# Kernel tuning notes

Measured on AMD Instinct MI355X. Metric: run time of the kernel, lower is better.

The kernel has to match this reference:

```python
import jax, jax.numpy as jnp
import numpy as np

B, S, DM = 1, 2048, 2048
H, KV, DH = 32, 8, 64
ROT, DQ = 32, 16  # rotary dims; DQ = ROT // 2
GROUPS = H // KV


def setup_inputs() -> dict:
    key = jax.random.key(0)
    ks = jax.random.split(key, 9)
    sc = 0.02
    hidden_states = jax.random.normal(ks[0], (B, S, DM), jnp.float32)
    # realistic RoPE tables: theta = pos * inv_freq, shape [1,1,S,DQ] (broadcasts over heads)
    inv_freq = 1.0 / (10000.0 ** (jnp.arange(DQ, dtype=jnp.float32) / DQ))
    ang = jnp.arange(S, dtype=jnp.float32)[:, None] * inv_freq[None, :]
    cos = jnp.cos(ang)[None, None]
    sin = jnp.sin(ang)[None, None]
    position_ids = jnp.broadcast_to(jnp.arange(S, dtype=jnp.int64 if jax.config.read('jax_enable_x64') else jnp.int32), (B, S))
    Wq = jax.random.normal(ks[1], (DM, H * DH), jnp.float32) * sc
    Wk = jax.random.normal(ks[2], (DM, KV * DH), jnp.float32) * sc
    Wv = jax.random.normal(ks[3], (DM, KV * DH), jnp.float32) * sc
    Wo = jax.random.normal(ks[4], (H * DH, DM), jnp.float32) * sc
    qkv_dim = H * DH + 2 * KV * DH
    tau_Wq = jax.random.normal(ks[5], (qkv_dim, H), jnp.float32) * sc
    tau_Wv = jax.random.normal(ks[6], (qkv_dim, H), jnp.float32) * sc
    tau_alpha = jax.random.normal(ks[7], (H,), jnp.float32)
    return {"hidden_states": hidden_states, "cos": cos, "sin": sin,
            "position_ids": position_ids, "Wq": Wq, "Wk": Wk, "Wv": Wv,
            "Wo": Wo, "tau_Wq": tau_Wq, "tau_Wv": tau_Wv, "tau_alpha": tau_alpha}


def _rope(x, cos, sin):
    # x: [B, h, S, DH]; rotate first ROT dims (half-split real/imag), interleave output
    x_rot, x_pass = x[..., :ROT], x[..., ROT:]
    xr, xi = x_rot[..., :DQ], x_rot[..., DQ:]
    out_r = xr * cos - xi * sin
    out_i = xr * sin + xi * cos
    out = jnp.stack([out_r, out_i], axis=-1).reshape(x.shape[:-1] + (ROT,))
    return jnp.concatenate([out, x_pass], axis=-1)


def reference(hidden_states, cos, sin, position_ids, Wq, Wk, Wv, Wo, tau_Wq, tau_Wv, tau_alpha):
    b, s, _ = hidden_states.shape
    q = hidden_states @ Wq                      # [B,S,H*DH]
    k = hidden_states @ Wk                      # [B,S,KV*DH]
    v = hidden_states @ Wv                      # [B,S,KV*DH]
    # tau gating: gelu(concat qkv) -> tanh projections -> position sigmoid term
    feat = jax.nn.gelu(jnp.concatenate([q, k, v], axis=-1), approximate=False)
    tok_q = jnp.tanh(feat @ tau_Wq).transpose(0, 2, 1)   # [B,H,S]
    tok_v = jnp.tanh(feat @ tau_Wv).transpose(0, 2, 1)   # [B,H,S]
    pos = position_ids.astype(hidden_states.dtype) + 1.0
    tau_pos = 1.0 + (jax.nn.sigmoid(tau_alpha[None, :, None] * jnp.log(pos)[:, None, :]) - 0.5)
    tau_q = (tok_q + tau_pos)[..., None]        # [B,H,S,1]
    tau_v = (tok_v + tau_pos)[..., None]        # [B,H,S,1]
    q = q.reshape(b, s, H, DH).transpose(0, 2, 1, 3) * tau_q   # [B,H,S,DH]
    k = k.reshape(b, s, KV, DH).transpose(0, 2, 1, 3)          # [B,KV,S,DH]
    # torch: tau_v.repeat(1,groups,1,1)[:, :KV] == first KV heads of tau_v
    v = v.reshape(b, s, KV, DH).transpose(0, 2, 1, 3) * tau_v[:, :KV]
    q = _rope(q, cos, sin)
    k = _rope(k, cos, sin)
    # GQA expand kv heads, causal SDPA
    k = jnp.repeat(k, GROUPS, axis=1)
    v = jnp.repeat(v, GROUPS, axis=1)
    scores = jnp.einsum('bhqd,bhkd->bhqk', q, k) / np.sqrt(DH).astype(np.float32)
    causal = jnp.tril(jnp.ones((s, s), dtype=bool))
    scores = jnp.where(causal, scores, jnp.finfo(scores.dtype).min)
    attn = jax.nn.softmax(scores, axis=-1)
    out = jnp.einsum('bhqk,bhkd->bhqd', attn, v)
    out = out.transpose(0, 2, 1, 3).reshape(b, s, H * DH)
    return out @ Wo
```

## Files before the change

kernel.cpp:

```cpp
#include <hip/hip_runtime.h>
#include <cmath>

typedef __bf16 bf16x8 __attribute__((ext_vector_type(8)));
typedef __bf16 bf16x4 __attribute__((ext_vector_type(4)));
typedef float f32x4 __attribute__((ext_vector_type(4)));
typedef short s16x4 __attribute__((ext_vector_type(4)));
typedef unsigned short u16;
typedef unsigned int u32;

__device__ __forceinline__ u16 f2bf(float f) {
  union { float f; unsigned int u; } v; v.f = f;
  unsigned int u = v.u;
  return (u16)((u + 0x7FFFu + ((u >> 16) & 1u)) >> 16);
}

__device__ __forceinline__ float geluf(float x) {
  return 0.5f * x * (1.0f + erff(x * 0.7071067811865475f));
}

__device__ __forceinline__ f32x4 mfma_16x16x16_bf16(s16x4 a, s16x4 b, f32x4 c) {
#if __has_builtin(__builtin_amdgcn_mfma_f32_16x16x16bf16_1k)
  return __builtin_amdgcn_mfma_f32_16x16x16bf16_1k(a, b, c, 0, 0, 0);
#else
  f32x4 d;
  asm volatile("v_mfma_f32_16x16x16_bf16 %0, %1, %2, %3"
               : "=v"(d) : "v"(a), "v"(b), "0"(c));
  return d;
#endif
}

__device__ __forceinline__ void gl_lds16(const void* g, void* l) {
  __builtin_amdgcn_global_load_lds(
      (const __attribute__((address_space(1))) u32*)g,
      (__attribute__((address_space(3))) u32*)l, 16, 0, 0);
}

__global__ __launch_bounds__(256) void cvt_bf16(const float* __restrict__ in,
                                                u16* __restrict__ out, int n8) {
  int i = blockIdx.x * 256 + threadIdx.x;
  if (i >= n8) return;
  const float4* p = (const float4*)in + 2 * (size_t)i;
  float4 a = p[0], b = p[1];
  uint4 o;
  o.x = (unsigned)f2bf(a.x) | ((unsigned)f2bf(a.y) << 16);
  o.y = (unsigned)f2bf(a.z) | ((unsigned)f2bf(a.w) << 16);
  o.z = (unsigned)f2bf(b.x) | ((unsigned)f2bf(b.y) << 16);
  o.w = (unsigned)f2bf(b.z) | ((unsigned)f2bf(b.w) << 16);
  ((uint4*)out)[i] = o;
}

__global__ __launch_bounds__(256) void transpose_all(const float* __restrict__ Wq,
                                                     const float* __restrict__ Wk,
                                                     const float* __restrict__ Wv,
                                                     const float* __restrict__ Wo,
                                                     const float* __restrict__ tWq,
                                                     const float* __restrict__ tWv,
                                                     u16* __restrict__ WqkvT,
                                                     u16* __restrict__ WoT,
                                                     u16* __restrict__ Tt) {
  __shared__ float tile[64][65];
  int b = blockIdx.x;
  const float* in; u16* out; int R, C, bx, by;
  if (b < 1024)      { in = Wq;  out = WqkvT;                R = 2048; C = 2048; bx = b & 31; by = b >> 5; }
  else if (b < 1280) { b -= 1024; in = Wk; out = WqkvT + 2048ull * 2048; R = 2048; C = 512; bx = b & 7; by = b >> 3; }
  else if (b < 1536) { b -= 1280; in = Wv; out = WqkvT + 2560ull * 2048; R = 2048; C = 512; bx = b & 7; by = b >> 3; }
  else if (b < 2560) { b -= 1536; in = Wo; out = WoT;        R = 2048; C = 2048; bx = b & 31; by = b >> 5; }
  else if (b < 2608) { b -= 2560; in = tWq; out = Tt;               R = 3072; C = 32; bx = 0; by = b; }
  else               { b -= 2608; in = tWv; out = Tt + 32ull * 3072; R = 3072; C = 32; bx = 0; by = b; }

  const int t = threadIdx.x;
  const int r0 = by * 64, c0 = bx * 64;
  const int lr = t >> 4, lc4 = (t & 15) * 4;
#pragma unroll
  for (int p = 0; p < 4; ++p) {
    int r = p * 16 + lr;
    float4 v = {0.f, 0.f, 0.f, 0.f};
    if (c0 + lc4 < C) v = *(const float4*)(in + (size_t)(r0 + r) * C + c0 + lc4);
    tile[r][lc4] = v.x; tile[r][lc4 + 1] = v.y;
    tile[r][lc4 + 2] = v.z; tile[r][lc4 + 3] = v.w;
  }
  __syncthreads();
  const int cg = t >> 4, rr4 = (t & 15) * 4;
#pragma unroll
  for (int p = 0; p < 4; ++p) {
    int c = p * 16 + cg;
    if (c0 + c < C) {
      uint2 w;
      w.x = (u32)f2bf(tile[rr4][c])     | ((u32)f2bf(tile[rr4 + 1][c]) << 16);
      w.y = (u32)f2bf(tile[rr4 + 2][c]) | ((u32)f2bf(tile[rr4 + 3][c]) << 16);
      *(uint2*)(out + (size_t)(c0 + c) * R + r0 + rr4) = w;
    }
  }
}

template <int WR, int WC>
__global__ __launch_bounds__(256, 3) void gemm_bt(const u16* __restrict__ A,
                                                  const u16* __restrict__ Bt,
                                                  float* __restrict__ Cpart,
                                                  int M, int N, int K, int kPer) {
  constexpr int BM = WR * 64, BN = WC * 64;
  __shared__ __attribute__((aligned(16))) u16 As[BM * 64];
  __shared__ __attribute__((aligned(16))) u16 Bs[BN * 64];
  const int tid = threadIdx.x, wid = tid >> 6, lane = tid & 63;
  const int l16 = lane & 15, quad = lane >> 4;
  const int wm = (wid % WR) * 64, wn = (wid / WR) * 64;
  const int m0 = blockIdx.y * BM, n0 = blockIdx.x * BN;
  const int kIters = K >> 6;
  const int kStart = blockIdx.z * kPer;
  const int kEnd = (kStart + kPer < kIters) ? (kStart + kPer) : kIters;

  const int lrow = lane >> 3;
  const int swz = (lane & 7) ^ lrow;
  const u16* gAb = A + (size_t)m0 * K + (size_t)swz * 8;
  const u16* gBb = Bt + (size_t)n0 * K + (size_t)swz * 8;
  const int sx = l16 & 7;

  f32x4 acc[4][4] = {};
  for (int kt = kStart; kt < kEnd; ++kt) {
    __syncthreads();
    const u16* gA = gAb + (size_t)kt * 64;
    const u16* gB = gBb + (size_t)kt * 64;
#pragma unroll
    for (int j = 0; j < BM / 32; ++j) {
      int i = wid * (BM / 32) + j;
      gl_lds16(gA + (size_t)(i * 8 + lrow) * K, &As[i * 512]);
    }
#pragma unroll
    for (int j = 0; j < BN / 32; ++j) {
      int i = wid * (BN / 32) + j;
      gl_lds16(gB + (size_t)(i * 8 + lrow) * K, &Bs[i * 512]);
    }
    __syncthreads();
    bf16x8 af[4][2], bfr[4][2];
#pragma unroll
    for (int mt = 0; mt < 4; ++mt)
#pragma unroll
      for (int ks = 0; ks < 2; ++ks)
        af[mt][ks] = *(const bf16x8*)(&As[(wm + mt * 16 + l16) * 64 +
                                          (((ks * 4 + quad) ^ sx) * 8)]);
#pragma unroll
    for (int nt = 0; nt < 4; ++nt)
#pragma unroll
      for (int ks = 0; ks < 2; ++ks)
        bfr[nt][ks] = *(const bf16x8*)(&Bs[(wn + nt * 16 + l16) * 64 +
                                           (((ks * 4 + quad) ^ sx) * 8)]);
#pragma unroll
    for (int mt = 0; mt < 4; ++mt)
#pragma unroll
      for (int nt = 0; nt < 4; ++nt)
#pragma unroll
        for (int ks = 0; ks < 2; ++ks)
          acc[mt][nt] = __builtin_amdgcn_mfma_f32_16x16x32_bf16(
              af[mt][ks], bfr[nt][ks], acc[mt][nt], 0, 0, 0);
  }

  float* C = Cpart + (size_t)blockIdx.z * M * N;
#pragma unroll
  for (int mt = 0; mt < 4; ++mt)
#pragma unroll
    for (int nt = 0; nt < 4; ++nt)
#pragma unroll
      for (int r = 0; r < 4; ++r) {
        int row = m0 + wm + mt * 16 + quad * 4 + r;
        int col = n0 + wn + nt * 16 + l16;
        C[(size_t)row * N + col] = acc[mt][nt][r];
      }
}

__global__ __launch_bounds__(256) void reduce_gelu(float* __restrict__ base, int P,
                                                   int n4, u16* __restrict__ gout) {
  int i = blockIdx.x * 256 + threadIdx.x;
  if (i >= n4) return;
  size_t n = (size_t)n4 * 4;
  float4 v = ((const float4*)base)[i];
  for (int p = 1; p < P; ++p) {
    float4 w = ((const float4*)(base + (size_t)p * n))[i];
    v.x += w.x; v.y += w.y; v.z += w.z; v.w += w.w;
  }
  if (P > 1) ((float4*)base)[i] = v;
  uint2 o;
  o.x = (u32)f2bf(geluf(v.x)) | ((u32)f2bf(geluf(v.y)) << 16);
  o.y = (u32)f2bf(geluf(v.z)) | ((u32)f2bf(geluf(v.w)) << 16);
  ((uint2*)gout)[i] = o;
}

__global__ __launch_bounds__(256) void reduce_add(const float* __restrict__ base, int P,
                                                  int n4, float* __restrict__ dst) {
  int i = blockIdx.x * 256 + threadIdx.x;
  if (i >= n4) return;
  size_t n = (size_t)n4 * 4;
  float4 v = ((const float4*)base)[i];
  for (int p = 1; p < P; ++p) {
    float4 w = ((const float4*)(base + (size_t)p * n))[i];
    v.x += w.x; v.y += w.y; v.z += w.z; v.w += w.w;
  }
  ((float4*)dst)[i] = v;
}

__global__ __launch_bounds__(256) void reduce_tanh(const float* __restrict__ base, int P,
                                                   int n, float* __restrict__ tokq,
                                                   float* __restrict__ tokv) {
  int i = blockIdx.x * 256 + threadIdx.x;
  if (i >= n) return;
  float v = base[i];
  for (int p = 1; p < P; ++p) v += base[(size_t)p * n + i];
  float t = tanhf(v);
  int col = i & 63, row = i >> 6;
  if (col < 32) tokq[row * 32 + col] = t;
  else          tokv[row * 32 + (col - 32)] = t;
}

#define QSCALE 0.18033688011112042f
__global__ __launch_bounds__(256) void prep_qkv(const float* __restrict__ qkv,
                                                const float* __restrict__ tokq,
                                                const float* __restrict__ tokv,
                                                const float* __restrict__ alpha,
                                                const float* __restrict__ cosb,
                                                const float* __restrict__ sinb,
                                                const int* __restrict__ pos_ids,
                                                u16* __restrict__ Qb,
                                                u16* __restrict__ Kb,
                                                u16* __restrict__ Vt,
                                                u16* __restrict__ Vb) {
  const int s = blockIdx.x;
  const int tid = threadIdx.x;
  __shared__ float cs[16], sn[16], tq_s[32], tv_s[32];
  if (tid < 16) { cs[tid] = cosb[s * 16 + tid]; sn[tid] = sinb[s * 16 + tid]; }
  if (tid < 32) {
    float p = (float)pos_ids[s] + 1.0f;
    float sig = 1.0f / (1.0f + __expf(-alpha[tid] * logf(p)));
    float taupos = 0.5f + sig;
    tq_s[tid] = (tokq[s * 32 + tid] + taupos) * QSCALE;
    tv_s[tid] = tokv[s * 32 + tid] + taupos;
  }
  __syncthreads();
  const float* row = qkv + (size_t)s * 3072;

  for (int idx = tid; idx < 2048; idx += 256) {
    int h = idx >> 6, d = idx & 63;
    float tq = tq_s[h];
    float v;
    if (d < 32) {
      int i = d >> 1;
      float xr = row[h * 64 + i] * tq, xi = row[h * 64 + 16 + i] * tq;
      v = (d & 1) ? (xr * sn[i] + xi * cs[i]) : (xr * cs[i] - xi * sn[i]);
    } else v = row[h * 64 + d] * tq;
    Qb[((size_t)h * 2048 + s) * 64 + d] = f2bf(v);
  }
  for (int idx = tid; idx < 512; idx += 256) {
    int h = idx >> 6, d = idx & 63;
    const float* kr = row + 2048;
    float v;
    if (d < 32) {
      int i = d >> 1;
      float xr = kr[h * 64 + i], xi = kr[h * 64 + 16 + i];
      v = (d & 1) ? (xr * sn[i] + xi * cs[i]) : (xr * cs[i] - xi * sn[i]);
    } else v = kr[h * 64 + d];
    Kb[((size_t)h * 2048 + s) * 64 + d] = f2bf(v);
  }
  for (int idx = tid; idx < 512; idx += 256) {
    int h = idx >> 6, d = idx & 63;
    float v = row[2560 + h * 64 + d] * tv_s[h];
    u16 b = f2bf(v);
    if (Vb) Vb[((size_t)h * 2048 + s) * 64 + d] = b;
    else    Vt[((size_t)h * 64 + d) * 2048 + s] = b;
  }
}

__global__ __launch_bounds__(256) void vtrans(const u16* __restrict__ Vb,
                                              u16* __restrict__ Vt) {
  __shared__ u16 t[64][68];
  const int s0 = blockIdx.x * 64, h = blockIdx.y;
  const int tid = threadIdx.x;
  const u16* src = Vb + ((size_t)h * 2048 + s0) * 64;
#pragma unroll
  for (int p = 0; p < 4; ++p) {
    int v = p * 256 + tid;
    int r = v >> 4, c = (v & 15) * 4;
    uint2 w = *(const uint2*)(src + (size_t)r * 64 + c);
    t[r][c] = (u16)(w.x & 0xffff); t[r][c + 1] = (u16)(w.x >> 16);
    t[r][c + 2] = (u16)(w.y & 0xffff); t[r][c + 3] = (u16)(w.y >> 16);
  }
  __syncthreads();
  u16* dst = Vt + (size_t)h * 64 * 2048 + s0;
#pragma unroll
  for (int p = 0; p < 4; ++p) {
    int v = p * 256 + tid;
    int d = v >> 4, s = (v & 15) * 4;
    uint2 w;
    w.x = (u32)t[s][d] | ((u32)t[s + 1][d] << 16);
    w.y = (u32)t[s + 2][d] | ((u32)t[s + 3][d] << 16);
    *(uint2*)(dst + (size_t)d * 2048 + s) = w;
  }
}

__global__ __launch_bounds__(256, 4) void flash_attn(const u16* __restrict__ Qb,
                                                     const u16* __restrict__ Kb,
                                                     const u16* __restrict__ Vt,
                                                     float* __restrict__ Opart,
                                                     float* __restrict__ ml) {
  __shared__ __attribute__((aligned(16))) u16 KsB[2][4096];
  __shared__ __attribute__((aligned(16))) u16 VsB[2][4096];
  const int e = 50 - blockIdx.x;
  const int h = blockIdx.y, kvh = h >> 2;
  int a = 0;
  while (3 * (a + 1) * (a + 2) / 2 <= e) ++a;
  const int rem = e - 3 * a * (a + 1) / 2;
  const int qb = 3 * a + rem / (a + 1);
  const int cc = rem % (a + 1);
  const int k0 = cc * 6;
  const int kvTend = 2 * qb + 2;
  const int k1 = (k0 + 6 < kvTend) ? (k0 + 6) : kvTend;
  const int pid = h * 51 + e;

  const int tid = threadIdx.x, wid = tid >> 6, lane = tid & 63;
  const int l16 = lane & 15, quad = lane >> 4;
  const int lrow = lane >> 3, swz = (lane & 7) ^ lrow, sx = l16 & 7;

  const int q0 = qb * 128 + wid * 32;
  bf16x8 qf[2][2];
#pragma unroll
  for (int mt = 0; mt < 2; ++mt)
#pragma unroll
    for (int ks = 0; ks < 2; ++ks)
      qf[mt][ks] = *(const bf16x8*)(Qb + ((size_t)h * 2048 + q0 + mt * 16 + l16) * 64 +
                                    ks * 32 + quad * 8);

  f32x4 oacc[2][4] = {};
  float mrun[2] = {-3e38f, -3e38f};
  float lrun[2] = {0.f, 0.f};

  const u16* kgb = Kb + ((size_t)kvh * 2048) * 64;
  const u16* vgb = Vt + (size_t)kvh * 64 * 2048;

#define FA_STAGE(KT, BUF)                                                         \
  {                                                                               \
    const u16* kg_ = kgb + (size_t)(KT)*64 * 64;                                  \
    const u16* vg_ = vgb + (size_t)(KT)*64;                                       \
    _Pragma("unroll") for (int j = 0; j < 2; ++j) {                               \
      int i_ = wid * 2 + j;                                                       \
      gl_lds16(kg_ + (size_t)(i_ * 8 + lrow) * 64 + swz * 8, &KsB[BUF][i_ * 512]);\
      gl_lds16(vg_ + (size_t)(i_ * 8 + lrow) * 2048 + swz * 8, &VsB[BUF][i_ * 512]);\
    }                                                                             \
  }

  FA_STAGE(k0, 0)
  for (int kt = k0; kt < k1; ++kt) {
    const int cur = (kt - k0) & 1;
    __syncthreads();
    if (kt + 1 < k1) FA_STAGE(kt + 1, cur ^ 1)
    const u16* Ks = KsB[cur];
    const u16* Vs = VsB[cur];

    f32x4 sacc[2][4] = {};
    __builtin_amdgcn_s_setprio(1);
#pragma unroll
    for (int kf = 0; kf < 4; ++kf) {
      bf16x8 a0 = *(const bf16x8*)(Ks + (kf * 16 + l16) * 64 + ((quad ^ sx) << 3));
      bf16x8 a1 = *(const bf16x8*)(Ks + (kf * 16 + l16) * 64 + (((4 + quad) ^ sx) << 3));
      sacc[0][kf] = __builtin_amdgcn_mfma_f32_16x16x32_bf16(a0, qf[0][0], sacc[0][kf], 0, 0, 0);
      sacc[0][kf] = __builtin_amdgcn_mfma_f32_16x16x32_bf16(a1, qf[0][1], sacc[0][kf], 0, 0, 0);
      sacc[1][kf] = __builtin_amdgcn_mfma_f32_16x16x32_bf16(a0, qf[1][0], sacc[1][kf], 0, 0, 0);
      sacc[1][kf] = __builtin_amdgcn_mfma_f32_16x16x32_bf16(a1, qf[1][1], sacc[1][kf], 0, 0, 0);
    }
    __builtin_amdgcn_s_setprio(0);

    const bool msk = (kt >= 2 * qb);
    s16x4 pb[2][4];
#pragma unroll
    for (int mt = 0; mt < 2; ++mt) {
      const int qg = q0 + mt * 16 + l16;
      if (msk) {
        const int kb = kt * 64 + quad * 4;
#pragma unroll
        for (int kf = 0; kf < 4; ++kf)
#pragma unroll
          for (int r = 0; r < 4; ++r)
            if (kb + kf * 16 + r > qg) sacc[mt][kf][r] = -1e9f;
      }
      f32x4 m4 = sacc[mt][0];
      m4 = __builtin_elementwise_max(m4, sacc[mt][1]);
      m4 = __builtin_elementwise_max(m4, sacc[mt][2]);
      m4 = __builtin_elementwise_max(m4, sacc[mt][3]);
      float mx = fmaxf(fmaxf(m4[0], m4[1]), fmaxf(m4[2], m4[3]));
      mx = fmaxf(mx, __shfl_xor(mx, 16));
      mx = fmaxf(mx, __shfl_xor(mx, 32));
      float mn = fmaxf(mrun[mt], mx);
      float al = __builtin_amdgcn_exp2f(mrun[mt] - mn);
      mrun[mt] = mn;
      float psl = 0.f;
#pragma unroll
      for (int kf = 0; kf < 4; ++kf) {
        bf16x4 ph;
#pragma unroll
        for (int r = 0; r < 4; ++r) {
          float p = __builtin_amdgcn_exp2f(sacc[mt][kf][r] - mn);
          psl += p;
          ph[r] = (__bf16)p;
        }
        union { bf16x4 h; s16x4 s; } cv;
        cv.h = ph;
        pb[mt][kf] = cv.s;
      }
      lrun[mt] = lrun[mt] * al + psl;
#pragma unroll
      for (int df = 0; df < 4; ++df) oacc[mt][df] *= al;
    }

    __builtin_amdgcn_s_setprio(1);
#pragma unroll
    for (int kf = 0; kf < 4; ++kf) {
#pragma unroll
      for (int df = 0; df < 4; ++df) {
        s16x4 va = *(const s16x4*)(Vs + (df * 16 + l16) * 64 +
                                   (((kf * 2 + (quad >> 1)) ^ sx) << 3) + ((quad & 1) << 2));
        oacc[0][df] = mfma_16x16x16_bf16(va, pb[0][kf], oacc[0][df]);
        oacc[1][df] = mfma_16x16x16_bf16(va, pb[1][kf], oacc[1][df]);
      }
    }
    __builtin_amdgcn_s_setprio(0);
  }
#undef FA_STAGE

  float* Op = Opart + (size_t)pid * 128 * 64;
#pragma unroll
  for (int mt = 0; mt < 2; ++mt) {
    float lt = lrun[mt];
    lt += __shfl_xor(lt, 16);
    lt += __shfl_xor(lt, 32);
    const int qrow = wid * 32 + mt * 16 + l16;
#pragma unroll
    for (int df = 0; df < 4; ++df)
      *(f32x4*)(Op + (size_t)qrow * 64 + df * 16 + quad * 4) = oacc[mt][df];
    if (quad == 0) {
      ml[((size_t)pid * 128 + qrow) * 2] = mrun[mt];
      ml[((size_t)pid * 128 + qrow) * 2 + 1] = lt;
    }
  }
}

__global__ __launch_bounds__(256) void fa_combine(const float* __restrict__ Opart,
                                                  const float* __restrict__ ml,
                                                  u16* __restrict__ Ob) {
  const int qb = blockIdx.x, h = blockIdx.y;
  const int C = (2 * qb + 7) / 6;
  const int aa = qb / 3, bb = qb % 3;
  const int base = h * 51 + 3 * aa * (aa + 1) / 2 + bb * (aa + 1);
  const int t = threadIdx.x;
#pragma unroll
  for (int u = 0; u < 8; ++u) {
    int unit = u * 256 + t;
    int row = unit >> 4, d4 = unit & 15;
    float mstar = -3e38f;
    for (int c = 0; c < C; ++c)
      mstar = fmaxf(mstar, ml[((size_t)(base + c) * 128 + row) * 2]);
    float4 o = {0.f, 0.f, 0.f, 0.f};
    float lsum = 0.f;
    for (int c = 0; c < C; ++c) {
      const float* mlp = &ml[((size_t)(base + c) * 128 + row) * 2];
      float w = __builtin_amdgcn_exp2f(mlp[0] - mstar);
      float4 v = ((const float4*)(Opart + ((size_t)(base + c) * 128 + row) * 64))[d4];
      o.x += w * v.x; o.y += w * v.y; o.z += w * v.z; o.w += w * v.w;
      lsum += w * mlp[1];
    }
    float inv = 1.0f / lsum;
    uint2 pk;
    pk.x = (u32)f2bf(o.x * inv) | ((u32)f2bf(o.y * inv) << 16);
    pk.y = (u32)f2bf(o.z * inv) | ((u32)f2bf(o.w * inv) << 16);
    *(uint2*)(Ob + (size_t)(qb * 128 + row) * 2048 + h * 64 + d4 * 4) = pk;
  }
}

extern "C" void kernel_launch(void* const* d_in, const int* in_sizes, int n_in,
                              void* d_out, int out_size, void* d_ws, size_t ws_size,
                              hipStream_t stream) {
  (void)in_sizes; (void)n_in; (void)out_size;
  const float* hidden = (const float*)d_in[0];
  const float* cosb   = (const float*)d_in[1];
  const float* sinb   = (const float*)d_in[2];
  const int*   pos    = (const int*)d_in[3];
  const float* Wq     = (const float*)d_in[4];
  const float* Wk     = (const float*)d_in[5];
  const float* Wv     = (const float*)d_in[6];
  const float* Wo     = (const float*)d_in[7];
  const float* tWq    = (const float*)d_in[8];
  const float* tWv    = (const float*)d_in[9];
  const float* alpha  = (const float*)d_in[10];
  float* out = (float*)d_out;

  const bool big = ws_size >= (size_t)120 * 1024 * 1024;
  const int Pq = big ? 2 : 1;
  const int Pt = big ? 16 : 1;
  const int Po = big ? 3 : 1;

  char* ws = (char*)d_ws;
  size_t off = 0;
  auto alloc = [&](size_t bytes) -> void* {
    void* p = ws + off;
    off += (bytes + 255) & ~(size_t)255;
    return p;
  };
  u16*   WoT   = (u16*)alloc(2048ull * 2048 * 2);
  u16*   Tt    = (u16*)alloc(64ull * 3072 * 2);
  u16*   Qb    = (u16*)alloc(32ull * 2048 * 64 * 2);
  u16*   Kb    = (u16*)alloc(8ull * 2048 * 64 * 2);
  u16*   Vt    = (u16*)alloc(8ull * 64 * 2048 * 2);
  u16*   Ob    = (u16*)alloc(2048ull * 2048 * 2);
  u16*   featb = (u16*)alloc(2048ull * 3072 * 2);
  float* tokq  = (float*)alloc(2048ull * 32 * 4);
  float* tokv  = (float*)alloc(2048ull * 32 * 4);
  u16*   Vb    = big ? (u16*)alloc(8ull * 2048 * 64 * 2) : nullptr;
  size_t E = off;
  u16*   Xb      = (u16*)alloc(2048ull * 2048 * 2);
  u16*   WqkvT   = (u16*)alloc(3072ull * 2048 * 2);
  float* qkvPart = (float*)alloc((size_t)Pq * 2048 * 3072 * 4);
  float* qkv     = qkvPart;
  float* tokPart = (float*)(ws + E);
  float* Opart   = (float*)(ws + E);
  float* mlbuf   = (float*)(ws + E + 1632ull * 128 * 64 * 4);
  float* outPart = (float*)(ws + E);

  cvt_bf16<<<2048, 256, 0, stream>>>(hidden, Xb, 2048 * 2048 / 8);
  transpose_all<<<2656, 256, 0, stream>>>(Wq, Wk, Wv, Wo, tWq, tWv, WqkvT, WoT, Tt);

  gemm_bt<2, 2><<<dim3(24, 16, Pq), 256, 0, stream>>>(
      Xb, WqkvT, qkvPart, 2048, 3072, 2048, (32 + Pq - 1) / Pq);
  reduce_gelu<<<6144, 256, 0, stream>>>(qkvPart, Pq, 2048 * 3072 / 4, featb);

  gemm_bt<4, 1><<<dim3(1, 8, Pt), 256, 0, stream>>>(
      featb, Tt, tokPart, 2048, 64, 3072, (48 + Pt - 1) / Pt);
  reduce_tanh<<<512, 256, 0, stream>>>(tokPart, Pt, 2048 * 64, tokq, tokv);

  prep_qkv<<<2048, 256, 0, stream>>>(qkv, tokq, tokv, alpha, cosb, sinb, pos,
                                     Qb, Kb, Vt, Vb);
  if (big) vtrans<<<dim3(32, 8), 256, 0, stream>>>(Vb, Vt);

  flash_attn<<<dim3(51, 32), 256, 0, stream>>>(Qb, Kb, Vt, Opart, mlbuf);
  fa_combine<<<dim3(16, 32), 256, 0, stream>>>(Opart, mlbuf, Ob);

  gemm_bt<2, 2><<<dim3(16, 16, Po), 256, 0, stream>>>(
      Ob, WoT, outPart, 2048, 2048, 2048, (32 + Po - 1) / Po);
  reduce_add<<<4096, 256, 0, stream>>>(outPart, Po, 2048 * 2048 / 4, out);
}
```

Measured before the change: 292.7 us.

## Single-buffer flash-attention K/V with split staging; store partials as bf16

Replaces the double-buffered K/V LDS tiles with single buffers. The next K tile is prefetched after the QK^T MFMAs and the next V tile after the PV MFMAs, with explicit vmcnt/lgkmcnt waits and barriers. This halves LDS use so the launch bounds can ask for 8 blocks per CU instead of 4. The partial attention outputs are written as bf16 instead of fp32 to cut combine traffic, at some precision cost, and the output GEMM split factor Po drops from 3 to 2. The extra barriers per iteration and the manual waitcnt counting could add stalls or be fragile.

```diff
diff --git a/kernel.cpp b/kernel.cpp
--- a/kernel.cpp
+++ b/kernel.cpp
@@ -12,6 +12,10 @@
   union { float f; unsigned int u; } v; v.f = f;
   unsigned int u = v.u;
   return (u16)((u + 0x7FFFu + ((u >> 16) & 1u)) >> 16);
+}
+
+__device__ __forceinline__ float bf2f(u16 b) {
+  union { u32 u; float f; } v; v.u = (u32)b << 16; return v.f;
 }
 
 __device__ __forceinline__ float geluf(float x) {
@@ -294,13 +298,13 @@
   }
 }
 
-__global__ __launch_bounds__(256, 4) void flash_attn(const u16* __restrict__ Qb,
+__global__ __launch_bounds__(256, 8) void flash_attn(const u16* __restrict__ Qb,
                                                      const u16* __restrict__ Kb,
                                                      const u16* __restrict__ Vt,
-                                                     float* __restrict__ Opart,
+                                                     u16* __restrict__ Opart,
                                                      float* __restrict__ ml) {
-  __shared__ __attribute__((aligned(16))) u16 KsB[2][4096];
-  __shared__ __attribute__((aligned(16))) u16 VsB[2][4096];
+  __shared__ __attribute__((aligned(16))) u16 Ks[4096];
+  __shared__ __attribute__((aligned(16))) u16 Vs[4096];
   const int e = 50 - blockIdx.x;
   const int h = blockIdx.y, kvh = h >> 2;
   int a = 0;
@@ -333,24 +337,31 @@
   const u16* kgb = Kb + ((size_t)kvh * 2048) * 64;
   const u16* vgb = Vt + (size_t)kvh * 64 * 2048;
 
-#define FA_STAGE(KT, BUF)                                                         \
-  {                                                                               \
-    const u16* kg_ = kgb + (size_t)(KT)*64 * 64;                                  \
-    const u16* vg_ = vgb + (size_t)(KT)*64;                                       \
-    _Pragma("unroll") for (int j = 0; j < 2; ++j) {                               \
-      int i_ = wid * 2 + j;                                                       \
-      gl_lds16(kg_ + (size_t)(i_ * 8 + lrow) * 64 + swz * 8, &KsB[BUF][i_ * 512]);\
-      gl_lds16(vg_ + (size_t)(i_ * 8 + lrow) * 2048 + swz * 8, &VsB[BUF][i_ * 512]);\
-    }                                                                             \
-  }
-
-  FA_STAGE(k0, 0)
+#define FA_STAGE_K(KT)                                                              \
+  {                                                                                 \
+    const u16* kg_ = kgb + (size_t)(KT)*64 * 64;                                    \
+    _Pragma("unroll") for (int j = 0; j < 2; ++j) {                                 \
+      int i_ = wid * 2 + j;                                                         \
+      gl_lds16(kg_ + (size_t)(i_ * 8 + lrow) * 64 + swz * 8, &Ks[i_ * 512]);        \
+    }                                                                               \
+  }
+#define FA_STAGE_V(KT)                                                              \
+  {                                                                                 \
+    const u16* vg_ = vgb + (size_t)(KT)*64;                                         \
+    _Pragma("unroll") for (int j = 0; j < 2; ++j) {                                 \
+      int i_ = wid * 2 + j;                                                         \
+      gl_lds16(vg_ + (size_t)(i_ * 8 + lrow) * 2048 + swz * 8, &Vs[i_ * 512]);      \
+    }                                                                               \
+  }
+#define FA_FENCE asm volatile("" ::: "memory")
+
+  FA_STAGE_K(k0)
+  FA_STAGE_V(k0)
   for (int kt = k0; kt < k1; ++kt) {
-    const int cur = (kt - k0) & 1;
-    __syncthreads();
-    if (kt + 1 < k1) FA_STAGE(kt + 1, cur ^ 1)
-    const u16* Ks = KsB[cur];
-    const u16* Vs = VsB[cur];
+    const bool pf = (kt + 1 < k1);
+    asm volatile("s_waitcnt vmcnt(2)" ::: "memory");
+    __builtin_amdgcn_s_barrier();
+    FA_FENCE;
 
     f32x4 sacc[2][4] = {};
     __builtin_amdgcn_s_setprio(1);
@@ -364,6 +375,11 @@
       sacc[1][kf] = __builtin_amdgcn_mfma_f32_16x16x32_bf16(a1, qf[1][1], sacc[1][kf], 0, 0, 0);
     }
     __builtin_amdgcn_s_setprio(0);
+
+    asm volatile("s_waitcnt lgkmcnt(0)" ::: "memory");
+    __builtin_amdgcn_s_barrier();
+    FA_FENCE;
+    if (pf) FA_STAGE_K(kt + 1)
 
     const bool msk = (kt >= 2 * qb);
     s16x4 pb[2][4];
@@ -407,6 +423,11 @@
       for (int df = 0; df < 4; ++df) oacc[mt][df] *= al;
     }
 
+    if (pf) { asm volatile("s_waitcnt vmcnt(2)" ::: "memory"); }
+    else    { asm volatile("s_waitcnt vmcnt(0)" ::: "memory"); }
+    __builtin_amdgcn_s_barrier();
+    FA_FENCE;
+
     __builtin_amdgcn_s_setprio(1);
 #pragma unroll
     for (int kf = 0; kf < 4; ++kf) {
@@ -419,10 +440,16 @@
       }
     }
     __builtin_amdgcn_s_setprio(0);
-  }
-#undef FA_STAGE
-
-  float* Op = Opart + (size_t)pid * 128 * 64;
+
+    asm volatile("s_waitcnt lgkmcnt(0)" ::: "memory");
+    __builtin_amdgcn_s_barrier();
+    FA_FENCE;
+    if (pf) FA_STAGE_V(kt + 1)
+  }
+#undef FA_STAGE_K
+#undef FA_STAGE_V
+
+  u16* Op = Opart + (size_t)pid * 128 * 64;
 #pragma unroll
   for (int mt = 0; mt < 2; ++mt) {
     float lt = lrun[mt];
@@ -430,8 +457,12 @@
     lt += __shfl_xor(lt, 32);
     const int qrow = wid * 32 + mt * 16 + l16;
 #pragma unroll
-    for (int df = 0; df < 4; ++df)
-      *(f32x4*)(Op + (size_t)qrow * 64 + df * 16 + quad * 4) = oacc[mt][df];
+    for (int df = 0; df < 4; ++df) {
+      uint2 pk2;
+      pk2.x = (u32)f2bf(oacc[mt][df][0]) | ((u32)f2bf(oacc[mt][df][1]) << 16);
+      pk2.y = (u32)f2bf(oacc[mt][df][2]) | ((u32)f2bf(oacc[mt][df][3]) << 16);
+      *(uint2*)(Op + (size_t)qrow * 64 + df * 16 + quad * 4) = pk2;
+    }
     if (quad == 0) {
       ml[((size_t)pid * 128 + qrow) * 2] = mrun[mt];
       ml[((size_t)pid * 128 + qrow) * 2 + 1] = lt;
@@ -439,7 +470,7 @@
   }
 }
 
-__global__ __launch_bounds__(256) void fa_combine(const float* __restrict__ Opart,
+__global__ __launch_bounds__(256) void fa_combine(const u16* __restrict__ Opart,
                                                   const float* __restrict__ ml,
                                                   u16* __restrict__ Ob) {
   const int qb = blockIdx.x, h = blockIdx.y;
@@ -459,8 +490,11 @@
     for (int c = 0; c < C; ++c) {
       const float* mlp = &ml[((size_t)(base + c) * 128 + row) * 2];
       float w = __builtin_amdgcn_exp2f(mlp[0] - mstar);
-      float4 v = ((const float4*)(Opart + ((size_t)(base + c) * 128 + row) * 64))[d4];
-      o.x += w * v.x; o.y += w * v.y; o.z += w * v.z; o.w += w * v.w;
+      uint2 v = *(const uint2*)(Opart + ((size_t)(base + c) * 128 + row) * 64 + d4 * 4);
+      o.x += w * bf2f((u16)(v.x & 0xffff));
+      o.y += w * bf2f((u16)(v.x >> 16));
+      o.z += w * bf2f((u16)(v.y & 0xffff));
+      o.w += w * bf2f((u16)(v.y >> 16));
       lsum += w * mlp[1];
     }
     float inv = 1.0f / lsum;
@@ -491,7 +525,7 @@
   const bool big = ws_size >= (size_t)120 * 1024 * 1024;
   const int Pq = big ? 2 : 1;
   const int Pt = big ? 16 : 1;
-  const int Po = big ? 3 : 1;
+  const int Po = big ? 2 : 1;
 
   char* ws = (char*)d_ws;
   size_t off = 0;
@@ -516,8 +550,8 @@
   float* qkvPart = (float*)alloc((size_t)Pq * 2048 * 3072 * 4);
   float* qkv     = qkvPart;
   float* tokPart = (float*)(ws + E);
-  float* Opart   = (float*)(ws + E);
-  float* mlbuf   = (float*)(ws + E + 1632ull * 128 * 64 * 4);
+  u16*   Opart   = (u16*)(ws + E);
+  float* mlbuf   = (float*)(ws + E + 1632ull * 128 * 64 * 2);
   float* outPart = (float*)(ws + E);
 
   cvt_bf16<<<2048, 256, 0, stream>>>(hidden, Xb, 2048 * 2048 / 8);
```

Measured after the change: 553.9 us. 89.2% more time.

## Store attention partials as bf16 via LDS staging, remap grid, retune out-proj split

Applied to the files above, without the earlier changes.

The flash-attention partial outputs are now packed to bf16 and staged through swizzled LDS, so each block writes them to global memory with coalesced 16-byte stores. The combine kernel reads and unpacks these bf16 partials. Halving the partial-buffer traffic cuts memory bandwidth between the attention and combine stages, at the cost of some precision in the unnormalized partial sums. The grid is flattened to 1D with heads interleaved so blocks sharing a KV head are scheduled together for better L2 reuse, and the output-projection split-K factor drops from 3 to 2.

```diff
diff --git a/kernel.cpp b/kernel.cpp
--- a/kernel.cpp
+++ b/kernel.cpp
@@ -12,6 +12,10 @@
   union { float f; unsigned int u; } v; v.f = f;
   unsigned int u = v.u;
   return (u16)((u + 0x7FFFu + ((u >> 16) & 1u)) >> 16);
+}
+
+__device__ __forceinline__ float bf2f(u16 b) {
+  union { u32 u; float f; } v; v.u = (u32)b << 16; return v.f;
 }
 
 __device__ __forceinline__ float geluf(float x) {
@@ -297,12 +301,14 @@
 __global__ __launch_bounds__(256, 4) void flash_attn(const u16* __restrict__ Qb,
                                                      const u16* __restrict__ Kb,
                                                      const u16* __restrict__ Vt,
-                                                     float* __restrict__ Opart,
+                                                     u16* __restrict__ Opart,
                                                      float* __restrict__ ml) {
   __shared__ __attribute__((aligned(16))) u16 KsB[2][4096];
   __shared__ __attribute__((aligned(16))) u16 VsB[2][4096];
-  const int e = 50 - blockIdx.x;
-  const int h = blockIdx.y, kvh = h >> 2;
+  const int bid = blockIdx.x;
+  const int h = (bid & 7) | (((bid >> 3) & 3) << 3);
+  const int e = 50 - (bid >> 5);
+  const int kvh = h >> 2;
   int a = 0;
   while (3 * (a + 1) * (a + 2) / 2 <= e) ++a;
   const int rem = e - 3 * a * (a + 1) / 2;
@@ -422,7 +428,8 @@
   }
 #undef FA_STAGE
 
-  float* Op = Opart + (size_t)pid * 128 * 64;
+  __syncthreads();
+  char* Ls = (char*)KsB;
 #pragma unroll
   for (int mt = 0; mt < 2; ++mt) {
     float lt = lrun[mt];
@@ -430,16 +437,30 @@
     lt += __shfl_xor(lt, 32);
     const int qrow = wid * 32 + mt * 16 + l16;
 #pragma unroll
-    for (int df = 0; df < 4; ++df)
-      *(f32x4*)(Op + (size_t)qrow * 64 + df * 16 + quad * 4) = oacc[mt][df];
+    for (int df = 0; df < 4; ++df) {
+      uint2 pk2;
+      pk2.x = (u32)f2bf(oacc[mt][df][0]) | ((u32)f2bf(oacc[mt][df][1]) << 16);
+      pk2.y = (u32)f2bf(oacc[mt][df][2]) | ((u32)f2bf(oacc[mt][df][3]) << 16);
+      int boff = qrow * 128 + ((df * 32 + quad * 8) ^ ((qrow & 7) << 4));
+      *(uint2*)(Ls + boff) = pk2;
+    }
     if (quad == 0) {
       ml[((size_t)pid * 128 + qrow) * 2] = mrun[mt];
       ml[((size_t)pid * 128 + qrow) * 2 + 1] = lt;
     }
   }
-}
-
-__global__ __launch_bounds__(256) void fa_combine(const float* __restrict__ Opart,
+  __syncthreads();
+  char* Op = (char*)(Opart + (size_t)pid * 128 * 64);
+#pragma unroll
+  for (int p = 0; p < 4; ++p) {
+    int off = p * 4096 + tid * 16;
+    int row = off >> 7, wb = off & 127;
+    uint4 v = *(const uint4*)(Ls + row * 128 + (wb ^ ((row & 7) << 4)));
+    *(uint4*)(Op + off) = v;
+  }
+}
+
+__global__ __launch_bounds__(256) void fa_combine(const u16* __restrict__ Opart,
                                                   const float* __restrict__ ml,
                                                   u16* __restrict__ Ob) {
   const int qb = blockIdx.x, h = blockIdx.y;
@@ -459,8 +480,11 @@
     for (int c = 0; c < C; ++c) {
       const float* mlp = &ml[((size_t)(base + c) * 128 + row) * 2];
       float w = __builtin_amdgcn_exp2f(mlp[0] - mstar);
-      float4 v = ((const float4*)(Opart + ((size_t)(base + c) * 128 + row) * 64))[d4];
-      o.x += w * v.x; o.y += w * v.y; o.z += w * v.z; o.w += w * v.w;
+      uint2 v = *(const uint2*)(Opart + ((size_t)(base + c) * 128 + row) * 64 + d4 * 4);
+      o.x += w * bf2f((u16)(v.x & 0xffff));
+      o.y += w * bf2f((u16)(v.x >> 16));
+      o.z += w * bf2f((u16)(v.y & 0xffff));
+      o.w += w * bf2f((u16)(v.y >> 16));
       lsum += w * mlp[1];
     }
     float inv = 1.0f / lsum;
@@ -491,7 +515,7 @@
   const bool big = ws_size >= (size_t)120 * 1024 * 1024;
   const int Pq = big ? 2 : 1;
   const int Pt = big ? 16 : 1;
-  const int Po = big ? 3 : 1;
+  const int Po = big ? 2 : 1;
 
   char* ws = (char*)d_ws;
   size_t off = 0;
@@ -516,8 +540,8 @@
   float* qkvPart = (float*)alloc((size_t)Pq * 2048 * 3072 * 4);
   float* qkv     = qkvPart;
   float* tokPart = (float*)(ws + E);
-  float* Opart   = (float*)(ws + E);
-  float* mlbuf   = (float*)(ws + E + 1632ull * 128 * 64 * 4);
+  u16*   Opart   = (u16*)(ws + E);
+  float* mlbuf   = (float*)(ws + E + 1632ull * 128 * 64 * 2);
   float* outPart = (float*)(ws + E);
 
   cvt_bf16<<<2048, 256, 0, stream>>>(hidden, Xb, 2048 * 2048 / 8);
@@ -535,7 +559,7 @@
                                      Qb, Kb, Vt, Vb);
   if (big) vtrans<<<dim3(32, 8), 256, 0, stream>>>(Vb, Vt);
 
-  flash_attn<<<dim3(51, 32), 256, 0, stream>>>(Qb, Kb, Vt, Opart, mlbuf);
+  flash_attn<<<1632, 256, 0, stream>>>(Qb, Kb, Vt, Opart, mlbuf);
   fa_combine<<<dim3(16, 32), 256, 0, stream>>>(Opart, mlbuf, Ob);
 
   gemm_bt<2, 2><<<dim3(16, 16, Po), 256, 0, stream>>>(
```

Result: no change. 293.1 us (+0.1%).
